# Kernel tuning notes

Hardware: AMD Instinct MI355X
Metric: run time of the kernel (lower is better)

The kernel has to match this reference:

```python
import jax, jax.numpy as jnp
import numpy as np

L, E, H, R = 6, 1024, 8, 33
DH = E // H
FF = 4 * E
B, S = 8, 512


def _layer_norm(x, g, b, eps=1e-5):
    m = jnp.mean(x, axis=-1, keepdims=True)
    v = jnp.mean(jnp.square(x - m), axis=-1, keepdims=True)
    return (x - m) * jax.lax.rsqrt(v + eps) * g + b


def setup_inputs() -> dict:
    key = jax.random.key(0)
    ks = jax.random.split(key, 24)
    rn = lambda k, shape, s=0.02: (jax.random.normal(k, shape, jnp.float32) * s)
    inp = {
        'enc_padded': jax.random.normal(ks[0], (B, S, E), jnp.float32),
        'relations': jax.random.randint(ks[1], (B, S, S), 0, R),
        'enc_lengths': jax.random.randint(ks[2], (B,), 1, S + 1),
        'Wq': rn(ks[3], (L, E, E)), 'bq': jnp.zeros((L, E), jnp.float32),
        'Wk': rn(ks[4], (L, E, E)), 'bk': jnp.zeros((L, E), jnp.float32),
        'Wv': rn(ks[5], (L, E, E)), 'bv': jnp.zeros((L, E), jnp.float32),
        'Wo': rn(ks[6], (L, E, E)), 'bo': jnp.zeros((L, E), jnp.float32),
        'rel_k': rn(ks[7], (L, R, DH)),
        'rel_v': rn(ks[8], (L, R, DH)),
        'W1': rn(ks[9], (L, E, FF)), 'b1': jnp.zeros((L, FF), jnp.float32),
        'W2': rn(ks[10], (L, FF, E)), 'b2': jnp.zeros((L, E), jnp.float32),
        'ln1_g': jnp.ones((L, E), jnp.float32), 'ln1_b': jnp.zeros((L, E), jnp.float32),
        'ln2_g': jnp.ones((L, E), jnp.float32), 'ln2_b': jnp.zeros((L, E), jnp.float32),
        'lnf_g': jnp.ones((E,), jnp.float32), 'lnf_b': jnp.zeros((E,), jnp.float32),
    }
    return inp


def reference(enc_padded, relations, enc_lengths, Wq, bq, Wk, bk, Wv, bv, Wo, bo,
              rel_k, rel_v, W1, b1, W2, b2, ln1_g, ln1_b, ln2_g, ln2_b, lnf_g, lnf_b):
    x = enc_padded  # [B,S,E]
    dt = x.dtype
    # attention mask: valid iff both query and key positions are within seq length
    pos = jnp.arange(S)
    valid = pos[None, :] < enc_lengths[:, None]            # [B,S]
    mask2d = valid[:, :, None] & valid[:, None, :]          # [B,S,S]
    # one-hot relation indicator, shared across layers (R=33 is small)
    rel_oh = jax.nn.one_hot(relations, R, dtype=dt)        # [B,S,S,R]
    scale = 1.0 / np.sqrt(DH).astype(np.float32)

    def split_heads(t):  # [B,S,E] -> [B,H,S,DH]
        return t.reshape(B, S, H, DH).transpose(0, 2, 1, 3)

    for l in range(L):
        # --- relation-aware self-attention (pre-LN sublayer) ---
        h = _layer_norm(x, ln1_g[l], ln1_b[l])
        q = split_heads(h @ Wq[l] + bq[l])
        k = split_heads(h @ Wk[l] + bk[l])
        v = split_heads(h @ Wv[l] + bv[l])
        scores = jnp.einsum('bhid,bhjd->bhij', q, k)
        # relation key bias: q_i . rel_k[rel[i,j]]  via small [B,H,S,R] GEMM + one-hot contraction
        qr = jnp.einsum('bhid,rd->bhir', q, rel_k[l])
        scores = (scores + jnp.einsum('bhir,bijr->bhij', qr, rel_oh)) * scale
        scores = jnp.where(mask2d[:, None], scores, jnp.asarray(-1e9, dt))
        attn = jax.nn.softmax(scores, axis=-1)              # [B,H,S,S]
        out = jnp.einsum('bhij,bhjd->bhid', attn, v)
        # relation value bias: sum_j attn_ij * rel_v[rel[i,j]]
        a_rel = jnp.einsum('bhij,bijr->bhir', attn, rel_oh)
        out = out + jnp.einsum('bhir,rd->bhid', a_rel, rel_v[l])
        out = out.transpose(0, 2, 1, 3).reshape(B, S, E) @ Wo[l] + bo[l]
        x = x + out
        # --- position-wise feed-forward (pre-LN sublayer) ---
        h2 = _layer_norm(x, ln2_g[l], ln2_b[l])
        x = x + (jax.nn.relu(h2 @ W1[l] + b1[l]) @ W2[l] + b2[l])
    return _layer_norm(x, lnf_g, lnf_b)
```

## Files before the change

### kernel.cpp

```cpp
#include <hip/hip_runtime.h>

#define LNUM 6
#define EDIM 1024
#define HNUM 8
#define DHD  128
#define RNUM 33
#define FFD  4096
#define BNUM 8
#define SLEN 512
#define TOK  (BNUM*SLEN)

typedef __attribute__((ext_vector_type(8))) short bf16x8;
typedef __attribute__((ext_vector_type(4))) float f32x4;
typedef unsigned short u16;
typedef unsigned int u32;

__device__ __forceinline__ u16 f2b(float f) {
  u32 u = __builtin_bit_cast(u32, f);
  u32 r = u + 0x7FFFu + ((u >> 16) & 1u);
  return (u16)(r >> 16);
}
__device__ __forceinline__ u32 pck(float a, float b) { return (u32)f2b(a) | ((u32)f2b(b) << 16); }

#define GL16(gp, lp) __builtin_amdgcn_global_load_lds(                        \
    (const __attribute__((address_space(1))) void*)(gp),                      \
    (__attribute__((address_space(3))) void*)(lp), 16, 0, 0)

template<int BF16OUT>
__global__ __launch_bounds__(256) void ln_kernel(const float* __restrict__ x,
                                                 const float* __restrict__ g,
                                                 const float* __restrict__ be,
                                                 void* __restrict__ o) {
  int row = blockIdx.x;
  int t = threadIdx.x;
  const float* xr = x + (size_t)row * EDIM;
  float4 xv = *reinterpret_cast<const float4*>(xr + t * 4);
  float s1 = xv.x + xv.y + xv.z + xv.w;
  float s2 = xv.x*xv.x + xv.y*xv.y + xv.z*xv.z + xv.w*xv.w;
#pragma unroll
  for (int off = 32; off >= 1; off >>= 1) {
    s1 += __shfl_down(s1, off, 64);
    s2 += __shfl_down(s2, off, 64);
  }
  __shared__ float r1[4], r2[4];
  if ((t & 63) == 0) { r1[t >> 6] = s1; r2[t >> 6] = s2; }
  __syncthreads();
  s1 = r1[0] + r1[1] + r1[2] + r1[3];
  s2 = r2[0] + r2[1] + r2[2] + r2[3];
  float mean = s1 * (1.0f / EDIM);
  float var  = s2 * (1.0f / EDIM) - mean * mean;
  float rstd = rsqrtf(var + 1e-5f);
  float4 gv = *reinterpret_cast<const float4*>(g + t * 4);
  float4 bv = *reinterpret_cast<const float4*>(be + t * 4);
  float o0 = (xv.x - mean) * rstd * gv.x + bv.x;
  float o1 = (xv.y - mean) * rstd * gv.y + bv.y;
  float o2 = (xv.z - mean) * rstd * gv.z + bv.z;
  float o3 = (xv.w - mean) * rstd * gv.w + bv.w;
  if (BF16OUT) {
    ushort4 ov; ov.x = f2b(o0); ov.y = f2b(o1); ov.z = f2b(o2); ov.w = f2b(o3);
    *reinterpret_cast<ushort4*>((u16*)o + (size_t)row * EDIM + t * 4) = ov;
  } else {
    *reinterpret_cast<float4*>((float*)o + (size_t)row * EDIM + t * 4) = make_float4(o0, o1, o2, o3);
  }
}

__global__ __launch_bounds__(256) void wtrans(const float* __restrict__ src0,
                                              u16* __restrict__ dst0,
                                              int Kd, int Nd, size_t sstride, size_t dstride) {
  __shared__ float Ts[32][33];
  const float* src = src0 + blockIdx.z * sstride;
  u16* dst = dst0 + blockIdx.z * dstride;
  int r0 = blockIdx.y * 32, c0 = blockIdx.x * 32;
  int ty = threadIdx.x >> 3, tx = threadIdx.x & 7;
  float4 v = *reinterpret_cast<const float4*>(src + (size_t)(r0 + ty) * Nd + c0 + tx * 4);
  Ts[ty][tx*4+0] = v.x; Ts[ty][tx*4+1] = v.y; Ts[ty][tx*4+2] = v.z; Ts[ty][tx*4+3] = v.w;
  __syncthreads();
  ushort4 o;
  o.x = f2b(Ts[tx*4+0][ty]); o.y = f2b(Ts[tx*4+1][ty]);
  o.z = f2b(Ts[tx*4+2][ty]); o.w = f2b(Ts[tx*4+3][ty]);
  *reinterpret_cast<ushort4*>(dst + (size_t)(c0 + ty) * Kd + r0 + tx * 4) = o;
}

__global__ __launch_bounds__(256) void relpack(const int* __restrict__ rel,
                                               unsigned char* __restrict__ out) {
  __shared__ int Ts[32][33];
  int bz = blockIdx.z;
  int r0 = blockIdx.y * 32, c0 = blockIdx.x * 32;
  int ty = threadIdx.x >> 3, tx = threadIdx.x & 7;
  const int* src = rel + (size_t)bz * SLEN * SLEN;
  int4 v = *reinterpret_cast<const int4*>(src + (size_t)(r0 + ty) * SLEN + c0 + tx * 4);
  Ts[ty][tx*4+0] = v.x; Ts[ty][tx*4+1] = v.y; Ts[ty][tx*4+2] = v.z; Ts[ty][tx*4+3] = v.w;
  __syncthreads();
  u32 o = (u32)(Ts[tx*4+0][ty] & 255) | ((u32)(Ts[tx*4+1][ty] & 255) << 8) |
          ((u32)(Ts[tx*4+2][ty] & 255) << 16) | ((u32)(Ts[tx*4+3][ty] & 255) << 24);
  *reinterpret_cast<u32*>(out + (size_t)bz * SLEN * SLEN + (size_t)(c0 + ty) * SLEN + r0 + tx * 4) = o;
}

template<int BIASMODE, int ACT, int RES, int OUTBF16>
__global__ __launch_bounds__(256) void gemm_bt(const u16* __restrict__ A,
                                               const u16* __restrict__ B,
                                               const float* __restrict__ bias0,
                                               const float* __restrict__ bias1,
                                               const float* __restrict__ res,
                                               void* __restrict__ Cv,
                                               int M, int N, int K) {
  __shared__ u16 As[128 * 64];
  __shared__ u16 Bs[128 * 64];
  int t = threadIdx.x;
  int l = t & 63, w = t >> 6;
  int wm = w & 1, wn = w >> 1;
  int m0 = blockIdx.y * 128, n0 = blockIdx.x * 128;
  f32x4 acc[4][4] = {};
  const u16* Agp = A + (size_t)(m0 + w * 32 + (l >> 3)) * K + (l & 7) * 8;
  const u16* Bgp = B + (size_t)(n0 + w * 32 + (l >> 3)) * K + (l & 7) * 8;
  u16* Alp = As + w * 4 * 512;
  u16* Blp = Bs + w * 4 * 512;
  for (int k0 = 0; k0 < K; k0 += 64) {
    __syncthreads();
#pragma unroll
    for (int u = 0; u < 4; ++u) {
      GL16(Agp + (size_t)(u * 8) * K + k0, Alp + u * 512);
      GL16(Bgp + (size_t)(u * 8) * K + k0, Blp + u * 512);
    }
    __syncthreads();
#pragma unroll
    for (int d4 = 0; d4 < 2; ++d4) {
      bf16x8 af[4];
#pragma unroll
      for (int fm = 0; fm < 4; ++fm) {
        int row = wm * 64 + fm * 16 + (l & 15);
        af[fm] = *reinterpret_cast<const bf16x8*>(As + row * 64 + (d4 * 4 + (l >> 4)) * 8);
      }
#pragma unroll
      for (int fn = 0; fn < 4; ++fn) {
        int row = wn * 64 + fn * 16 + (l & 15);
        bf16x8 bf = *reinterpret_cast<const bf16x8*>(Bs + row * 64 + (d4 * 4 + (l >> 4)) * 8);
#pragma unroll
        for (int fm = 0; fm < 4; ++fm)
          acc[fm][fn] = __builtin_amdgcn_mfma_f32_16x16x32_bf16(af[fm], bf, acc[fm][fn], 0, 0, 0);
      }
    }
  }
#pragma unroll
  for (int fm = 0; fm < 4; ++fm)
#pragma unroll
    for (int fn = 0; fn < 4; ++fn)
#pragma unroll
      for (int e = 0; e < 4; ++e) {
        int m = m0 + wm * 64 + fm * 16 + (l >> 4) * 4 + e;
        int n = n0 + wn * 64 + fn * 16 + (l & 15);
        float v = acc[fm][fn][e];
        if (BIASMODE == 0) v += bias0[n];
        if (BIASMODE == 1) v += bias0[m];
        if (BIASMODE == 2) v += (n < 1024) ? bias0[n] : bias1[n - 1024];
        if (ACT == 1) v = fmaxf(v, 0.f);
        if (RES == 1) v += res[(size_t)m * N + n];
        if (OUTBF16) ((u16*)Cv)[(size_t)m * N + n] = f2b(v);
        else ((float*)Cv)[(size_t)m * N + n] = v;
      }
}

#define A_P  0
#define A_Q  16384
#define A_PS 32768
#define A_QR 40960
#define A_AR 50176
#define A_LS 59392
#define A_SM 59648

#define WAITVM4 do { asm volatile("s_waitcnt vmcnt(4)" ::: "memory"); \
                     __builtin_amdgcn_sched_barrier(0); } while (0)
#define WAITVM0 do { asm volatile("s_waitcnt vmcnt(0)" ::: "memory"); \
                     __builtin_amdgcn_sched_barrier(0); } while (0)

__global__ __launch_bounds__(256, 2) void attn_kernel(const u16* __restrict__ qk,
                                                      const u16* __restrict__ vt,
                                                      const unsigned char* __restrict__ rel8,
                                                      const int* __restrict__ lens,
                                                      const float* __restrict__ relk,
                                                      const float* __restrict__ relv,
                                                      u16* __restrict__ outb) {
  __align__(16) __shared__ char sm[A_SM];
  char*  Pb  = sm + A_P;
  char*  Qb  = sm + A_Q;
  char*  PSb = sm + A_PS;
  float* QR  = (float*)(sm + A_QR);
  float* AREL = (float*)(sm + A_AR);
  float* LSUM = (float*)(sm + A_LS);

  const int t = threadIdx.x;
  const int l = t & 63, w = t >> 6;
  const int lg = l >> 4;
  const int ll = l & 15;
  const int bx = blockIdx.x;
  const int xcd = bx & 7, rem = bx >> 3, slot = rem & 7, it = rem >> 3;
  const int g = slot * 8 + xcd;
  const int b = g >> 3, hh = g & 7;
  const int i0 = it * 64;
  const int len = lens[b];
  const float scale = 0.08838834764831845f;
  char* PSw = PSb + w * 2048;

  auto issueK = [&](int kt) {
#pragma unroll
    for (int u = 0; u < 4; ++u) {
      int row = w * 16 + u * 4 + (lg);
      int sb = (ll * 16) ^ (((u * 4 + lg) & 7) << 4);
      const u16* gp = qk + (size_t)(b * SLEN + kt * 64 + row) * 2048 + 1024 + hh * DHD + (sb >> 1);
      GL16(gp, Pb + (w * 4 + u) * 1024);
    }
  };
  auto issueV = [&](int kt) {
#pragma unroll
    for (int u = 0; u < 4; ++u) {
      int row = w * 32 + u * 8 + (l >> 3);
      int sb = ((l & 7) * 16) ^ ((l >> 3) << 4);
      const u16* gp = vt + (size_t)(hh * DHD + row) * TOK + b * SLEN + kt * 64 + (sb >> 1);
      GL16(gp, Qb + (w * 4 + u) * 1024);
    }
  };

  u32 relw[4];
  const unsigned char* relbase = rel8 + (size_t)b * SLEN * SLEN + (i0 + w * 16 + lg * 4);
  {
    const unsigned char* rb = relbase + (size_t)ll * SLEN;
#pragma unroll
    for (int fj = 0; fj < 4; ++fj)
      relw[fj] = *reinterpret_cast<const u32*>(rb + (size_t)(fj * 16) * SLEN);
  }
  for (int idx = l; idx < 16 * 36; idx += 64) AREL[w * 16 * 36 + idx] = 0.f;
  if (t < 192) {
    int r = t >> 2, sub = t & 3;
#pragma unroll
    for (int u = 0; u < 4; ++u) {
      int seg = sub * 4 + u;
      uint4 o;
      if (r < RNUM) {
        float4 f0 = *reinterpret_cast<const float4*>(relk + r * DHD + seg * 8);
        float4 f1 = *reinterpret_cast<const float4*>(relk + r * DHD + seg * 8 + 4);
        o.x = pck(f0.x, f0.y); o.y = pck(f0.z, f0.w);
        o.z = pck(f1.x, f1.y); o.w = pck(f1.z, f1.w);
      } else { o.x = o.y = o.z = o.w = 0u; }
      *reinterpret_cast<uint4*>(Pb + r * 256 + ((seg * 16) ^ ((r & 7) << 4))) = o;
    }
  }
  bf16x8 aq[4];
  {
    const u16* qrow = qk + (size_t)(b * SLEN + i0 + w * 16 + ll) * 2048 + hh * DHD;
#pragma unroll
    for (int d4 = 0; d4 < 4; ++d4)
      aq[d4] = *reinterpret_cast<const bf16x8*>(qrow + (d4 * 4 + lg) * 8);
  }
  __syncthreads();
#pragma unroll
  for (int rb = 0; rb < 3; ++rb) {
    f32x4 acc = {};
#pragma unroll
    for (int d4 = 0; d4 < 4; ++d4) {
      int rr = rb * 16 + ll;
      bf16x8 br = *reinterpret_cast<const bf16x8*>(Pb + rr * 256 + (((d4 * 4 + lg) * 16) ^ ((rr & 7) << 4)));
      acc = __builtin_amdgcn_mfma_f32_16x16x32_bf16(aq[d4], br, acc, 0, 0, 0);
    }
    int col = rb * 16 + ll;
    if (col < 36)
#pragma unroll
      for (int e = 0; e < 4; ++e)
        QR[(w * 16 + lg * 4 + e) * 36 + col] = acc[e];
  }
  __syncthreads();
  issueK(0);

  bool rowv[4];
#pragma unroll
  for (int e = 0; e < 4; ++e) rowv[e] = (i0 + w * 16 + lg * 4 + e) < len;

  float m_[4], ls_[4];
#pragma unroll
  for (int e = 0; e < 4; ++e) { m_[e] = -3.0e38f; ls_[e] = 0.f; }
  f32x4 oacc[8] = {};

  for (int kt = 0; kt < 8; ++kt) {
    issueV(kt);
    WAITVM4;
    __builtin_amdgcn_s_barrier();
    __builtin_amdgcn_s_setprio(1);
    f32x4 sacc[4];
#pragma unroll
    for (int fj = 0; fj < 4; ++fj) {
      f32x4 a = {};
#pragma unroll
      for (int d4 = 0; d4 < 4; ++d4) {
        int row = fj * 16 + ll;
        bf16x8 bk_ = *reinterpret_cast<const bf16x8*>(Pb + row * 256 + (((d4 * 4 + lg) * 16) ^ ((row & 7) << 4)));
        a = __builtin_amdgcn_mfma_f32_16x16x32_bf16(aq[d4], bk_, a, 0, 0, 0);
      }
      sacc[fj] = a;
    }
    __builtin_amdgcn_s_setprio(0);
    float pmax[4] = {-3.0e38f, -3.0e38f, -3.0e38f, -3.0e38f};
#pragma unroll
    for (int fj = 0; fj < 4; ++fj) {
      bool colv = (kt * 64 + fj * 16 + ll) < len;
      u32 rw = relw[fj];
#pragma unroll
      for (int e = 0; e < 4; ++e) {
        int r = (rw >> (8 * e)) & 255;
        float s = (sacc[fj][e] + QR[(w * 16 + lg * 4 + e) * 36 + r]) * scale;
        s = (rowv[e] && colv) ? s : -1e9f;
        sacc[fj][e] = s;
        pmax[e] = fmaxf(pmax[e], s);
      }
    }
#pragma unroll
    for (int e = 0; e < 4; ++e) {
      pmax[e] = fmaxf(pmax[e], __shfl_xor(pmax[e], 1, 64));
      pmax[e] = fmaxf(pmax[e], __shfl_xor(pmax[e], 2, 64));
      pmax[e] = fmaxf(pmax[e], __shfl_xor(pmax[e], 4, 64));
      pmax[e] = fmaxf(pmax[e], __shfl_xor(pmax[e], 8, 64));
    }
    float f_[4];
#pragma unroll
    for (int e = 0; e < 4; ++e) {
      float mn = fmaxf(m_[e], pmax[e]);
      f_[e] = __expf(m_[e] - mn);
      m_[e] = mn;
      ls_[e] *= f_[e];
    }
#pragma unroll
    for (int fd = 0; fd < 8; ++fd)
#pragma unroll
      for (int e = 0; e < 4; ++e) oacc[fd][e] *= f_[e];
#pragma unroll
    for (int e = 0; e < 4; ++e) {
      if (f_[e] != 1.0f) {
        int row = w * 16 + lg * 4 + e;
        AREL[row * 36 + ll] *= f_[e];
        AREL[row * 36 + 16 + ll] *= f_[e];
        if (ll == 0) AREL[row * 36 + 32] *= f_[e];
      }
    }
    float psum[4] = {0.f, 0.f, 0.f, 0.f};
#pragma unroll
    for (int fj = 0; fj < 4; ++fj) {
      u32 rw = relw[fj];
#pragma unroll
      for (int e = 0; e < 4; ++e) {
        float p = __expf(sacc[fj][e] - m_[e]);
        psum[e] += p;
        int iloc = lg * 4 + e;
        atomicAdd(&AREL[(w * 16 + iloc) * 36 + ((rw >> (8 * e)) & 255)], p);
        *reinterpret_cast<u16*>(PSw + iloc * 128 + (((fj * 16 + ll) * 2) ^ ((iloc & 7) << 4))) = f2b(p);
      }
    }
#pragma unroll
    for (int e = 0; e < 4; ++e) {
      psum[e] += __shfl_xor(psum[e], 1, 64);
      psum[e] += __shfl_xor(psum[e], 2, 64);
      psum[e] += __shfl_xor(psum[e], 4, 64);
      psum[e] += __shfl_xor(psum[e], 8, 64);
      ls_[e] += psum[e];
    }
    if (kt < 7) {
      const unsigned char* rb = relbase + (size_t)((kt + 1) * 64 + ll) * SLEN;
#pragma unroll
      for (int fj = 0; fj < 4; ++fj)
        relw[fj] = *reinterpret_cast<const u32*>(rb + (size_t)(fj * 16) * SLEN);
    }
    __builtin_amdgcn_s_barrier();
    if (kt < 7) issueK(kt + 1);
    if (kt < 7) { WAITVM4; } else { WAITVM0; }
    __builtin_amdgcn_s_barrier();
    __builtin_amdgcn_s_setprio(1);
#pragma unroll
    for (int kc = 0; kc < 2; ++kc) {
      bf16x8 pa = *reinterpret_cast<const bf16x8*>(PSw + ll * 128 + (((kc * 4 + lg) * 16) ^ ((ll & 7) << 4)));
#pragma unroll
      for (int fd = 0; fd < 8; ++fd) {
        int row = fd * 16 + ll;
        bf16x8 vb = *reinterpret_cast<const bf16x8*>(Qb + row * 128 + (((kc * 4 + lg) * 16) ^ ((row & 7) << 4)));
        oacc[fd] = __builtin_amdgcn_mfma_f32_16x16x32_bf16(pa, vb, oacc[fd], 0, 0, 0);
      }
    }
    __builtin_amdgcn_s_setprio(0);
    __builtin_amdgcn_s_barrier();
  }
#pragma unroll
  for (int e = 0; e < 4; ++e) {
    float inv = 1.0f / ls_[e];
#pragma unroll
    for (int fd = 0; fd < 8; ++fd) oacc[fd][e] *= inv;
  }
  if (ll == 0)
#pragma unroll
    for (int e = 0; e < 4; ++e) LSUM[w * 16 + lg * 4 + e] = ls_[e];
  for (int idx = t; idx < 128 * 64; idx += 256) {
    int d = idx >> 6, r = idx & 63;
    u16 v = (r < RNUM) ? f2b(relv[r * DHD + d]) : (u16)0;
    *reinterpret_cast<u16*>(Pb + d * 128 + ((r * 2) ^ ((d & 7) << 4))) = v;
  }
  for (int idx = l; idx < 1024; idx += 64) {
    int ri = idx >> 6, r = idx & 63;
    int row = w * 16 + ri;
    float v = (r < RNUM) ? AREL[row * 36 + r] * (1.0f / LSUM[row]) : 0.f;
    *reinterpret_cast<u16*>(PSw + ri * 128 + ((r * 2) ^ ((ri & 7) << 4))) = f2b(v);
  }
  __syncthreads();
#pragma unroll
  for (int kc = 0; kc < 2; ++kc) {
    bf16x8 pa = *reinterpret_cast<const bf16x8*>(PSw + ll * 128 + (((kc * 4 + lg) * 16) ^ ((ll & 7) << 4)));
#pragma unroll
    for (int fd = 0; fd < 8; ++fd) {
      int row = fd * 16 + ll;
      bf16x8 vb = *reinterpret_cast<const bf16x8*>(Pb + row * 128 + (((kc * 4 + lg) * 16) ^ ((row & 7) << 4)));
      oacc[fd] = __builtin_amdgcn_mfma_f32_16x16x32_bf16(pa, vb, oacc[fd], 0, 0, 0);
    }
  }
  char* OSw = Qb + w * 4096;
#pragma unroll
  for (int fd = 0; fd < 8; ++fd)
#pragma unroll
    for (int e = 0; e < 4; ++e)
      *reinterpret_cast<u16*>(OSw + ((lg * 4 + e) * 128 + fd * 16 + ll) * 2) = f2b(oacc[fd][e]);
  __syncthreads();
  {
    int ri = l >> 2, q4 = l & 3;
    const char* srcb = OSw + ri * 256 + q4 * 64;
    u16* dst = outb + (size_t)(b * SLEN + i0 + w * 16 + ri) * EDIM + hh * DHD + q4 * 32;
    uint4 x0 = *reinterpret_cast<const uint4*>(srcb);
    uint4 x1 = *reinterpret_cast<const uint4*>(srcb + 16);
    uint4 x2 = *reinterpret_cast<const uint4*>(srcb + 32);
    uint4 x3 = *reinterpret_cast<const uint4*>(srcb + 48);
    *reinterpret_cast<uint4*>(dst)      = x0;
    *reinterpret_cast<uint4*>(dst + 8)  = x1;
    *reinterpret_cast<uint4*>(dst + 16) = x2;
    *reinterpret_cast<uint4*>(dst + 24) = x3;
  }
}

extern "C" void kernel_launch(void* const* d_in, const int* in_sizes, int n_in,
                              void* d_out, int out_size, void* d_ws, size_t ws_size,
                              hipStream_t stream) {
  const float* enc  = (const float*)d_in[0];
  const int*   rel  = (const int*)d_in[1];
  const int*   lens = (const int*)d_in[2];
  const float* Wq = (const float*)d_in[3];
  const float* bq = (const float*)d_in[4];
  const float* Wk = (const float*)d_in[5];
  const float* bk = (const float*)d_in[6];
  const float* Wv = (const float*)d_in[7];
  const float* bv = (const float*)d_in[8];
  const float* Wo = (const float*)d_in[9];
  const float* bo = (const float*)d_in[10];
  const float* relk = (const float*)d_in[11];
  const float* relv = (const float*)d_in[12];
  const float* W1 = (const float*)d_in[13];
  const float* b1 = (const float*)d_in[14];
  const float* W2 = (const float*)d_in[15];
  const float* b2 = (const float*)d_in[16];
  const float* ln1g = (const float*)d_in[17];
  const float* ln1b = (const float*)d_in[18];
  const float* ln2g = (const float*)d_in[19];
  const float* ln2b = (const float*)d_in[20];
  const float* lnfg = (const float*)d_in[21];
  const float* lnfb = (const float*)d_in[22];
  float* out = (float*)d_out;

  char* W = (char*)d_ws;
  u16* h     = (u16*)W;
  unsigned char* rel8 = (unsigned char*)W;
  char* U    = W + 8388608;
  u16* qkb   = (u16*)U;
  u16* vtb   = (u16*)(U + 16777216);
  u16* attno = (u16*)(U + 25165824);
  u16* mid   = (u16*)U;
  bool xin = ws_size >= (size_t)83886080;
  float* x = xin ? (float*)(W + 41943040) : out;
  char* WT = W + (xin ? 58720256 : 41943040);
  bool big = ws_size >= (size_t)209715200;

  const size_t EE = (size_t)EDIM * EDIM;
  const size_t EF = (size_t)EDIM * FFD;

  u16 *WqkT, *WvT, *WoT, *W1T, *W2T;
  dim3 blk(256);
  if (big) {
    u16* wqk_all = (u16*)WT;
    u16* wv_all  = wqk_all + 6 * 2 * EE;
    u16* wo_all  = wv_all + 6 * EE;
    u16* w1_all  = wo_all + 6 * EE;
    u16* w2_all  = w1_all + 6 * EF;
    wtrans<<<dim3(32, 32, 6), blk, 0, stream>>>(Wq, wqk_all, 1024, 1024, EE, 2 * EE);
    wtrans<<<dim3(32, 32, 6), blk, 0, stream>>>(Wk, wqk_all + EE, 1024, 1024, EE, 2 * EE);
    wtrans<<<dim3(32, 32, 6), blk, 0, stream>>>(Wv, wv_all, 1024, 1024, EE, EE);
    wtrans<<<dim3(32, 32, 6), blk, 0, stream>>>(Wo, wo_all, 1024, 1024, EE, EE);
    wtrans<<<dim3(128, 32, 6), blk, 0, stream>>>(W1, w1_all, 1024, 4096, EF, EF);
    wtrans<<<dim3(32, 128, 6), blk, 0, stream>>>(W2, w2_all, 4096, 1024, EF, EF);
    WqkT = wqk_all; WvT = wv_all; WoT = wo_all; W1T = w1_all; W2T = w2_all;
  } else {
    WqkT = (u16*)WT;
    WvT  = WqkT + 2 * EE;
    WoT  = WvT + EE;
    W1T  = WoT + EE;
    W2T  = W1T + EF;
  }

  dim3 gLN(TOK);
  for (int ll = 0; ll < LNUM; ++ll) {
    u16 *wqkT, *wvT, *woT, *w1T, *w2T;
    if (big) {
      wqkT = WqkT + (size_t)ll * 2 * EE; wvT = WvT + (size_t)ll * EE; woT = WoT + (size_t)ll * EE;
      w1T = W1T + (size_t)ll * EF; w2T = W2T + (size_t)ll * EF;
    } else {
      wqkT = WqkT; wvT = WvT; woT = WoT; w1T = W1T; w2T = W2T;
      wtrans<<<dim3(32, 32, 1), blk, 0, stream>>>(Wq + ll * EE, wqkT, 1024, 1024, 0, 0);
      wtrans<<<dim3(32, 32, 1), blk, 0, stream>>>(Wk + ll * EE, wqkT + EE, 1024, 1024, 0, 0);
      wtrans<<<dim3(32, 32, 1), blk, 0, stream>>>(Wv + ll * EE, wvT, 1024, 1024, 0, 0);
      wtrans<<<dim3(32, 32, 1), blk, 0, stream>>>(Wo + ll * EE, woT, 1024, 1024, 0, 0);
      wtrans<<<dim3(128, 32, 1), blk, 0, stream>>>(W1 + ll * EF, w1T, 1024, 4096, 0, 0);
      wtrans<<<dim3(32, 128, 1), blk, 0, stream>>>(W2 + ll * EF, w2T, 4096, 1024, 0, 0);
    }
    const float* xin_p = (ll == 0) ? enc : x;
    ln_kernel<1><<<gLN, blk, 0, stream>>>(xin_p, ln1g + ll * EDIM, ln1b + ll * EDIM, h);
    gemm_bt<2, 0, 0, 1><<<dim3(16, 32), blk, 0, stream>>>(h, wqkT, bq + ll * EDIM, bk + ll * EDIM,
                                                          nullptr, qkb, TOK, 2048, EDIM);
    gemm_bt<1, 0, 0, 1><<<dim3(32, 8), blk, 0, stream>>>(wvT, h, bv + ll * EDIM, nullptr,
                                                         nullptr, vtb, EDIM, TOK, EDIM);
    relpack<<<dim3(16, 16, 8), blk, 0, stream>>>(rel, rel8);
    attn_kernel<<<dim3(512), blk, 0, stream>>>(qkb, vtb, rel8, lens,
                                               relk + (size_t)ll * RNUM * DHD,
                                               relv + (size_t)ll * RNUM * DHD, attno);
    gemm_bt<0, 0, 1, 0><<<dim3(8, 32), blk, 0, stream>>>(attno, woT, bo + ll * EDIM, nullptr,
                                                         xin_p, x, TOK, EDIM, EDIM);
    ln_kernel<1><<<gLN, blk, 0, stream>>>(x, ln2g + ll * EDIM, ln2b + ll * EDIM, h);
    gemm_bt<0, 1, 0, 1><<<dim3(32, 32), blk, 0, stream>>>(h, w1T, b1 + ll * FFD, nullptr,
                                                          nullptr, mid, TOK, FFD, EDIM);
    gemm_bt<0, 0, 1, 0><<<dim3(8, 32), blk, 0, stream>>>(mid, w2T, b2 + ll * EDIM, nullptr,
                                                         x, x, TOK, EDIM, FFD);
  }
  ln_kernel<0><<<gLN, blk, 0, stream>>>(x, lnfg, lnfb, out);
}
```

Measured before the change: 2.296 ms.

## Lazy softmax rescale, derive row sums from relation histogram, swizzle GEMM tiles

The attention kernel now skips the cross-lane max reduction and rescaling of the accumulators unless some row max exceeds the running max by more than a threshold (lazy rescale). The per-row softmax denominator is recovered at the end by summing the relation-bucket accumulator AREL rather than keeping a separately shuffled running sum. The GEMM kernel also remaps block IDs with an XCD-style swizzle so tiles that share operands land near each other. These remove per-tile shuffles and multiplies but allow exp values up to e^8 before rescaling, and rely on the AREL sums exactly covering all probabilities.

```diff
diff --git a/kernel.cpp b/kernel.cpp
--- a/kernel.cpp
+++ b/kernel.cpp
@@ -109,7 +109,11 @@
   int t = threadIdx.x;
   int l = t & 63, w = t >> 6;
   int wm = w & 1, wn = w >> 1;
-  int m0 = blockIdx.y * 128, n0 = blockIdx.x * 128;
+  int nwg = gridDim.x * gridDim.y;
+  int bid = blockIdx.y * gridDim.x + blockIdx.x;
+  int cpx = nwg >> 3;
+  int swz = (bid & 7) * cpx + (bid >> 3);
+  int m0 = (swz / gridDim.x) * 128, n0 = (swz % gridDim.x) * 128;
   f32x4 acc[4][4] = {};
   const u16* Agp = A + (size_t)(m0 + w * 32 + (l >> 3)) * K + (l & 7) * 8;
   const u16* Bgp = B + (size_t)(n0 + w * 32 + (l >> 3)) * K + (l & 7) * 8;
@@ -274,9 +278,9 @@
 #pragma unroll
   for (int e = 0; e < 4; ++e) rowv[e] = (i0 + w * 16 + lg * 4 + e) < len;
 
-  float m_[4], ls_[4];
-#pragma unroll
-  for (int e = 0; e < 4; ++e) { m_[e] = -3.0e38f; ls_[e] = 0.f; }
+  float m_[4];
+#pragma unroll
+  for (int e = 0; e < 4; ++e) m_[e] = -3.0e38f;
   f32x4 oacc[8] = {};
 
   for (int kt = 0; kt < 8; ++kt) {
@@ -297,7 +301,6 @@
       sacc[fj] = a;
     }
     __builtin_amdgcn_s_setprio(0);
-    float pmax[4] = {-3.0e38f, -3.0e38f, -3.0e38f, -3.0e38f};
 #pragma unroll
     for (int fj = 0; fj < 4; ++fj) {
       bool colv = (kt * 64 + fj * 16 + ll) < len;
@@ -308,57 +311,45 @@
         float s = (sacc[fj][e] + QR[(w * 16 + lg * 4 + e) * 36 + r]) * scale;
         s = (rowv[e] && colv) ? s : -1e9f;
         sacc[fj][e] = s;
-        pmax[e] = fmaxf(pmax[e], s);
-      }
-    }
-#pragma unroll
-    for (int e = 0; e < 4; ++e) {
-      pmax[e] = fmaxf(pmax[e], __shfl_xor(pmax[e], 1, 64));
-      pmax[e] = fmaxf(pmax[e], __shfl_xor(pmax[e], 2, 64));
-      pmax[e] = fmaxf(pmax[e], __shfl_xor(pmax[e], 4, 64));
-      pmax[e] = fmaxf(pmax[e], __shfl_xor(pmax[e], 8, 64));
-    }
-    float f_[4];
-#pragma unroll
-    for (int e = 0; e < 4; ++e) {
-      float mn = fmaxf(m_[e], pmax[e]);
-      f_[e] = __expf(m_[e] - mn);
-      m_[e] = mn;
-      ls_[e] *= f_[e];
-    }
-#pragma unroll
-    for (int fd = 0; fd < 8; ++fd)
-#pragma unroll
-      for (int e = 0; e < 4; ++e) oacc[fd][e] *= f_[e];
-#pragma unroll
-    for (int e = 0; e < 4; ++e) {
-      if (f_[e] != 1.0f) {
-        int row = w * 16 + lg * 4 + e;
-        AREL[row * 36 + ll] *= f_[e];
-        AREL[row * 36 + 16 + ll] *= f_[e];
-        if (ll == 0) AREL[row * 36 + 32] *= f_[e];
-      }
-    }
-    float psum[4] = {0.f, 0.f, 0.f, 0.f};
+      }
+    }
+    float pl[4];
+#pragma unroll
+    for (int e = 0; e < 4; ++e)
+      pl[e] = fmaxf(fmaxf(sacc[0][e], sacc[1][e]), fmaxf(sacc[2][e], sacc[3][e]));
+    bool ok = (pl[0] <= m_[0] + 8.f) && (pl[1] <= m_[1] + 8.f) &&
+              (pl[2] <= m_[2] + 8.f) && (pl[3] <= m_[3] + 8.f);
+    if (!__all(ok)) {
+#pragma unroll
+      for (int e = 0; e < 4; ++e) {
+        float px = pl[e];
+        px = fmaxf(px, __shfl_xor(px, 1, 64));
+        px = fmaxf(px, __shfl_xor(px, 2, 64));
+        px = fmaxf(px, __shfl_xor(px, 4, 64));
+        px = fmaxf(px, __shfl_xor(px, 8, 64));
+        float mn = fmaxf(m_[e], px);
+        float f = __expf(m_[e] - mn);
+        m_[e] = mn;
+#pragma unroll
+        for (int fd = 0; fd < 8; ++fd) oacc[fd][e] *= f;
+        if (f != 1.0f) {
+          int row = w * 16 + lg * 4 + e;
+          AREL[row * 36 + ll] *= f;
+          AREL[row * 36 + 16 + ll] *= f;
+          if (ll == 0) AREL[row * 36 + 32] *= f;
+        }
+      }
+    }
 #pragma unroll
     for (int fj = 0; fj < 4; ++fj) {
       u32 rw = relw[fj];
 #pragma unroll
       for (int e = 0; e < 4; ++e) {
         float p = __expf(sacc[fj][e] - m_[e]);
-        psum[e] += p;
         int iloc = lg * 4 + e;
         atomicAdd(&AREL[(w * 16 + iloc) * 36 + ((rw >> (8 * e)) & 255)], p);
         *reinterpret_cast<u16*>(PSw + iloc * 128 + (((fj * 16 + ll) * 2) ^ ((iloc & 7) << 4))) = f2b(p);
       }
-    }
-#pragma unroll
-    for (int e = 0; e < 4; ++e) {
-      psum[e] += __shfl_xor(psum[e], 1, 64);
-      psum[e] += __shfl_xor(psum[e], 2, 64);
-      psum[e] += __shfl_xor(psum[e], 4, 64);
-      psum[e] += __shfl_xor(psum[e], 8, 64);
-      ls_[e] += psum[e];
     }
     if (kt < 7) {
       const unsigned char* rb = relbase + (size_t)((kt + 1) * 64 + ll) * SLEN;
@@ -384,15 +375,18 @@
     __builtin_amdgcn_s_setprio(0);
     __builtin_amdgcn_s_barrier();
   }
+  if (l < 16) {
+    int row = w * 16 + l;
+    float s = 0.f;
+    for (int r = 0; r < RNUM; ++r) s += AREL[row * 36 + r];
+    LSUM[row] = s;
+  }
 #pragma unroll
   for (int e = 0; e < 4; ++e) {
-    float inv = 1.0f / ls_[e];
+    float inv = 1.0f / LSUM[w * 16 + lg * 4 + e];
 #pragma unroll
     for (int fd = 0; fd < 8; ++fd) oacc[fd][e] *= inv;
   }
-  if (ll == 0)
-#pragma unroll
-    for (int e = 0; e < 4; ++e) LSUM[w * 16 + lg * 4 + e] = ls_[e];
   for (int idx = t; idx < 128 * 64; idx += 256) {
     int d = idx >> 6, r = idx & 63;
     u16 v = (r < RNUM) ? f2b(relv[r * DHD + d]) : (u16)0;
```

Measured after the change: 2.297 ms. No clear change (+0.0%).
